# Kernel optimization log

Hardware: AMD Instinct MI355X
Metric: run time of the kernel (lower is better)

The kernel has to match this reference:

```python
import jax, jax.numpy as jnp
import numpy as np

INPUT_DIM, HIDDEN, CB_DIM, CB_SIZE = 768, 512, 256, 512
COMMIT_W = 1.0


def setup_inputs() -> dict:
    key = jax.random.key(0)
    ks = jax.random.split(key, 10)
    def lin(k, fan_in, fan_out):
        lim = 1.0 / np.sqrt(fan_in)
        return jax.random.uniform(k, (fan_in, fan_out), jnp.float32, -lim, lim)
    return {
        "x": jax.random.normal(ks[0], (32, 2048, INPUT_DIM), jnp.float32),
        "W1": lin(ks[1], INPUT_DIM, HIDDEN),
        "b1": jnp.zeros((HIDDEN,), jnp.float32),
        "W2": lin(ks[2], HIDDEN, CB_DIM),
        "b2": jnp.zeros((CB_DIM,), jnp.float32),
        "codebook": jax.random.normal(ks[3], (CB_SIZE, CB_DIM), jnp.float32),
        "W3": lin(ks[4], CB_DIM, HIDDEN),
        "b3": jnp.zeros((HIDDEN,), jnp.float32),
        "W4": lin(ks[5], HIDDEN, INPUT_DIM),
        "b4": jnp.zeros((INPUT_DIM,), jnp.float32),
    }


def reference(x, W1, b1, W2, b2, codebook, W3, b3, W4, b4):
    # encoder MLP: [b, n, 768] -> [b, n, 256]
    h = jax.nn.relu(jnp.einsum('bnd,dh->bnh', x, W1) + b1)
    z = jnp.einsum('bnh,hc->bnc', h, W2) + b2

    # VQ: squared-L2 distance to codebook, argmin, gather
    # d(z, c) = ||z||^2 - 2 z.c + ||c||^2  (||z||^2 constant over argmin, omitted)
    dots = jnp.einsum('bnc,kc->bnk', z, codebook)          # [b, n, K]
    c_sq = jnp.sum(codebook * codebook, axis=-1)            # [K]
    indices = jnp.argmin(c_sq - 2.0 * dots, axis=-1)        # [b, n] int
    q = codebook[indices]                                   # [b, n, 256] gather

    # straight-through estimator + commitment loss
    quantized = z + jax.lax.stop_gradient(q - z)
    commit_loss = COMMIT_W * jnp.mean((z - jax.lax.stop_gradient(q)) ** 2)

    # decoder MLP: [b, n, 256] -> [b, n, 768]
    h2 = jax.nn.relu(jnp.einsum('bnc,ch->bnh', quantized, W3) + b3)
    recon = jnp.einsum('bnh,hd->bnd', h2, W4) + b4
    return recon, indices.astype(jnp.int32), commit_loss
```

## Files before the change

### kernel.cpp

```cpp
#include <hip/hip_runtime.h>

typedef unsigned short u16;
typedef unsigned int   u32;
typedef __attribute__((ext_vector_type(8))) short short8;
typedef __attribute__((ext_vector_type(4))) float f32x4;

#define NTOK 65536
#define IND  768
#define HID  512
#define CBD  256
#define CBS  512

#define OUT_IDX_OFF   ((size_t)NTOK * IND)
#define OUT_LOSS_OFF  (OUT_IDX_OFF + NTOK)

#define OFF_H      ((size_t)0)
#define OFF_Z      ((size_t)134217728)
#define OFF_W1H    ((size_t)201326592)
#define OFF_W1L    ((size_t)202113024)
#define OFF_W2H    ((size_t)202899456)
#define OFF_W2L    ((size_t)203161600)
#define OFF_CBH    ((size_t)203423744)
#define OFF_CBL    ((size_t)203685888)
#define OFF_CSQ    ((size_t)203948032)
#define OFF_PART   ((size_t)0)
#define OFF_TABLE  ((size_t)8388608)
#define OFF_ZSQ    ((size_t)9961472)
#define OFF_IDX    ((size_t)10223616)
#define OFF_FLAGS  ((size_t)10485760)
#define OFF_CNT    ((size_t)10747904)

__device__ __forceinline__ u16 f2bf(float f) {
    u32 u = __float_as_uint(f);
    return (u16)((u + 0x7fffu + ((u >> 16) & 1u)) >> 16);
}
__device__ __forceinline__ float bf2f(u16 h) {
    return __uint_as_float(((u32)h) << 16);
}

__global__ __launch_bounds__(256) void cbsplit(
    const float* __restrict__ cb, u16* __restrict__ hi, u16* __restrict__ lo,
    float* __restrict__ csq)
{
    int c = blockIdx.x, t = threadIdx.x;
    float v = cb[(size_t)c * CBD + t];
    u16 h = f2bf(v); u16 l = f2bf(v - bf2f(h));
    hi[(size_t)c * CBD + t] = h; lo[(size_t)c * CBD + t] = l;
    __shared__ float red[256];
    red[t] = v * v; __syncthreads();
    for (int s = 128; s; s >>= 1) { if (t < s) red[t] += red[t + s]; __syncthreads(); }
    if (!t) csq[c] = red[0];
}

__global__ __launch_bounds__(256) void wsplit(
    const float* __restrict__ W, u16* __restrict__ hi, u16* __restrict__ lo,
    int K, int N)
{
    int n = blockIdx.x;
    for (int k = threadIdx.x; k < K; k += 256) {
        float v = W[(size_t)k * N + n];
        u16 h = f2bf(v); u16 l = f2bf(v - bf2f(h));
        hi[(size_t)n * K + k] = h; lo[(size_t)n * K + k] = l;
    }
}

#define CHS 1040
#define PLN (4 * CHS)

template<int AMODE, int EPI>
__global__ __launch_bounds__(256, 2) void gemm3(
    const float* __restrict__ Af, const u32* __restrict__ Apk,
    const u16* __restrict__ Bhi, const u16* __restrict__ Blo,
    const float* __restrict__ bias,
    u32* __restrict__ Opk, float* __restrict__ Opart,
    int M, int N, int K)
{
    __shared__ u16 lds[4 * PLN];
    u16* sAh = lds;
    u16* sAl = lds + PLN;
    u16* sBh = lds + 2 * PLN;
    u16* sBl = lds + 3 * PLN;
    const int tid  = threadIdx.x;

    const int nwg = gridDim.x * gridDim.y;
    const int hw  = blockIdx.y * gridDim.x + blockIdx.x;
    const int logical = (hw & 7) * (nwg >> 3) + (hw >> 3);
    const int bx = logical % gridDim.x;
    const int by = logical / gridDim.x;

    const int m0 = by * 128, n0 = bx * 128;
    const int w = tid >> 6, lane = tid & 63, quad = lane >> 4, l15 = lane & 15;
    const int wm = (w & 1) * 64, wn = (w >> 1) * 64;

    f32x4 acc[4][4] = {};

    for (int k0 = 0; k0 < K; k0 += 32) {
        __syncthreads();
        if (AMODE == 0) {
            #pragma unroll
            for (int s = 0; s < 4; ++s) {
                int slot = tid + s * 256;
                int m = slot >> 3, kg = (slot & 7) << 2;
                int c = kg >> 3, off = kg & 7;
                float4 v = *(const float4*)(Af + (size_t)(m0 + m) * K + k0 + kg);
                u16 h0 = f2bf(v.x), h1 = f2bf(v.y), h2 = f2bf(v.z), h3 = f2bf(v.w);
                ushort4 hv = {h0, h1, h2, h3};
                ushort4 lv = {f2bf(v.x - bf2f(h0)), f2bf(v.y - bf2f(h1)),
                              f2bf(v.z - bf2f(h2)), f2bf(v.w - bf2f(h3))};
                *(ushort4*)&sAh[c * CHS + m * 8 + off] = hv;
                *(ushort4*)&sAl[c * CHS + m * 8 + off] = lv;
            }
        } else {
            #pragma unroll
            for (int s = 0; s < 4; ++s) {
                int slot = tid + s * 256;
                int m = slot >> 3, ke = (slot & 7) << 2;
                int c = ke >> 3, off = ke & 7;
                uint4 u = *(const uint4*)(Apk + (size_t)(m0 + m) * K + k0 + ke);
                ushort4 hv = {(u16)(u.x & 0xffff), (u16)(u.y & 0xffff),
                              (u16)(u.z & 0xffff), (u16)(u.w & 0xffff)};
                ushort4 lv = {(u16)(u.x >> 16), (u16)(u.y >> 16),
                              (u16)(u.z >> 16), (u16)(u.w >> 16)};
                *(ushort4*)&sAh[c * CHS + m * 8 + off] = hv;
                *(ushort4*)&sAl[c * CHS + m * 8 + off] = lv;
            }
        }
        #pragma unroll
        for (int s = 0; s < 4; ++s) {
            int slot = tid + s * 256;
            int n = (slot & 511) >> 2, ku = slot & 3;
            const u16* src = (slot < 512) ? Bhi : Blo;
            u16* dst = (slot < 512) ? sBh : sBl;
            uint4 u = *(const uint4*)(src + (size_t)(n0 + n) * K + k0 + ku * 8);
            *(uint4*)&dst[ku * CHS + n * 8] = u;
        }
        __syncthreads();

        short8 ah[4], al[4], bh[4], bl[4];
        const int kc = quad * CHS;
        #pragma unroll
        for (int i = 0; i < 4; ++i) {
            int ar = wm + i * 16 + l15;
            int br = wn + i * 16 + l15;
            ah[i] = *(const short8*)&sAh[kc + ar * 8];
            al[i] = *(const short8*)&sAl[kc + ar * 8];
            bh[i] = *(const short8*)&sBh[kc + br * 8];
            bl[i] = *(const short8*)&sBl[kc + br * 8];
        }
        #pragma unroll
        for (int i = 0; i < 4; ++i)
            #pragma unroll
            for (int j = 0; j < 4; ++j) {
                acc[i][j] = __builtin_amdgcn_mfma_f32_16x16x32_bf16(ah[i], bh[j], acc[i][j], 0, 0, 0);
                acc[i][j] = __builtin_amdgcn_mfma_f32_16x16x32_bf16(ah[i], bl[j], acc[i][j], 0, 0, 0);
                acc[i][j] = __builtin_amdgcn_mfma_f32_16x16x32_bf16(al[i], bh[j], acc[i][j], 0, 0, 0);
            }
    }

    if (EPI <= 1) {
        float bn[4];
        #pragma unroll
        for (int j = 0; j < 4; ++j) bn[j] = bias[n0 + wn + j * 16 + l15];
        #pragma unroll
        for (int i = 0; i < 4; ++i)
            #pragma unroll
            for (int r = 0; r < 4; ++r) {
                int row = m0 + wm + i * 16 + quad * 4 + r;
                #pragma unroll
                for (int j = 0; j < 4; ++j) {
                    float v = acc[i][j][r] + bn[j];
                    if (EPI == 0) v = fmaxf(v, 0.f);
                    u16 h = f2bf(v); u16 l = f2bf(v - bf2f(h));
                    Opk[(size_t)row * N + n0 + wn + j * 16 + l15] = (u32)h | ((u32)l << 16);
                }
            }
    } else {
        float cs[4]; int cidx[4];
        #pragma unroll
        for (int j = 0; j < 4; ++j) {
            cidx[j] = n0 + wn + j * 16 + l15;
            cs[j] = bias[cidx[j]];
        }
        const int nparts = gridDim.x * 2;
        const int pslot  = bx * 2 + (w >> 1);
        #pragma unroll
        for (int i = 0; i < 4; ++i)
            #pragma unroll
            for (int r = 0; r < 4; ++r) {
                int row = m0 + wm + i * 16 + quad * 4 + r;
                float d1 = 3.4e38f, d2 = 3.4e38f; int i1 = 0x7fffffff;
                #pragma unroll
                for (int j = 0; j < 4; ++j) {
                    float v = fmaf(-2.0f, acc[i][j][r], cs[j]);
                    if (v < d1) { d2 = d1; d1 = v; i1 = cidx[j]; }
                    else d2 = fminf(d2, v);
                }
                #pragma unroll
                for (int mm = 1; mm < 16; mm <<= 1) {
                    float od1 = __shfl_xor(d1, mm, 64);
                    float od2 = __shfl_xor(d2, mm, 64);
                    int   oi1 = __shfl_xor(i1, mm, 64);
                    if (od1 < d1 || (od1 == d1 && oi1 < i1)) { d2 = fminf(d1, od2); d1 = od1; i1 = oi1; }
                    else d2 = fminf(d2, od1);
                }
                if (l15 == 0) {
                    float4 o = {d1, d2, __int_as_float(i1), 0.f};
                    *(float4*)&Opart[((size_t)row * nparts + pslot) * 4] = o;
                }
            }
    }
}

__global__ __launch_bounds__(256) void zsq_pk(
    const u32* __restrict__ Zpk, float* __restrict__ zsq)
{
    int tok = blockIdx.x * 4 + (threadIdx.x >> 6);
    int lane = threadIdx.x & 63;
    uint4 u = *(const uint4*)(Zpk + (size_t)tok * CBD + lane * 4);
    float z0 = bf2f((u16)(u.x & 0xffff)) + bf2f((u16)(u.x >> 16));
    float z1 = bf2f((u16)(u.y & 0xffff)) + bf2f((u16)(u.y >> 16));
    float z2 = bf2f((u16)(u.z & 0xffff)) + bf2f((u16)(u.z >> 16));
    float z3 = bf2f((u16)(u.w & 0xffff)) + bf2f((u16)(u.w >> 16));
    float s = z0 * z0 + z1 * z1 + z2 * z2 + z3 * z3;
    #pragma unroll
    for (int off = 32; off; off >>= 1) s += __shfl_down(s, off, 64);
    if (!lane) zsq[tok] = s;
}

__global__ __launch_bounds__(256) void vq_reduce(
    const float* __restrict__ part, const float* __restrict__ zsq,
    float* __restrict__ out_idx, int* __restrict__ idx_i,
    int* __restrict__ cnt, float* __restrict__ accum, int* __restrict__ flags)
{
    int tok = blockIdx.x * 256 + threadIdx.x;
    float d1 = 3.4e38f, d2 = 3.4e38f; int i1 = 0x7fffffff;
    #pragma unroll
    for (int nb = 0; nb < 8; ++nb) {
        float4 p = *(const float4*)&part[((size_t)tok * 8 + nb) * 4];
        float pd1 = p.x, pd2 = p.y; int pi1 = __float_as_int(p.z);
        if (pd1 < d1 || (pd1 == d1 && pi1 < i1)) { d2 = fminf(d1, pd2); d1 = pd1; i1 = pi1; }
        else d2 = fminf(d2, pd1);
    }
    out_idx[tok] = (float)i1;
    idx_i[tok] = i1;
    if (d2 - d1 < 0.01f) {
        int p = atomicAdd(cnt, 1);
        if (p >= 0 && p < NTOK) flags[p] = tok;
    }
    float c = zsq[tok] + d1;
    __shared__ float red[256];
    red[threadIdx.x] = c; __syncthreads();
    for (int s = 128; s; s >>= 1) { if (threadIdx.x < s) red[threadIdx.x] += red[threadIdx.x + s]; __syncthreads(); }
    if (!threadIdx.x) atomicAdd(accum, red[0]);
}

__global__ __launch_bounds__(256) void fixup(
    const int* __restrict__ cnt, const int* __restrict__ flags,
    const float* __restrict__ x, const float* __restrict__ W1, const float* __restrict__ b1,
    const float* __restrict__ W2, const float* __restrict__ b2,
    const float* __restrict__ cb, const float* __restrict__ csq,
    int* __restrict__ idx_i, float* __restrict__ out_idx)
{
    __shared__ float xs[8][IND];
    __shared__ float hs[8][HID];
    __shared__ float zs[8][CBD];
    __shared__ float bd_s[4][8];
    __shared__ int   bi_s[4][8];
    __shared__ int   tok_s[8];

    int n = cnt[0]; if (n > NTOK) n = NTOK; if (n < 0) n = 0;
    const int t = threadIdx.x;
    const int nb = (n + 7) >> 3;

    for (int ib = blockIdx.x; ib < nb; ib += gridDim.x) {
        const int base = ib * 8;
        if (t < 8) {
            int fi = base + t; if (fi > n - 1) fi = n - 1;
            tok_s[t] = flags[fi];
        }
        __syncthreads();

        #pragma unroll
        for (int s = 0; s < 6; ++s) {
            int slot = t + s * 256;
            int tt = slot / 192, c4 = slot - tt * 192;
            *(float4*)&xs[tt][c4 * 4] =
                *(const float4*)(x + (size_t)tok_s[tt] * IND + c4 * 4);
        }
        __syncthreads();

        {
            const int tg = t >> 7;
            const int j0 = (t & 127) * 4;
            float a[4][4];
            float4 bb = *(const float4*)(b1 + j0);
            #pragma unroll
            for (int ti = 0; ti < 4; ++ti) {
                a[ti][0] = bb.x; a[ti][1] = bb.y; a[ti][2] = bb.z; a[ti][3] = bb.w;
            }
            for (int k4 = 0; k4 < IND / 4; ++k4) {
                float4 xv[4];
                #pragma unroll
                for (int ti = 0; ti < 4; ++ti)
                    xv[ti] = *(const float4*)&xs[tg * 4 + ti][k4 * 4];
                #pragma unroll
                for (int kk = 0; kk < 4; ++kk) {
                    float4 wv = *(const float4*)(W1 + (size_t)(k4 * 4 + kk) * HID + j0);
                    #pragma unroll
                    for (int ti = 0; ti < 4; ++ti) {
                        float xk = (kk == 0) ? xv[ti].x : (kk == 1) ? xv[ti].y
                                 : (kk == 2) ? xv[ti].z : xv[ti].w;
                        a[ti][0] = fmaf(xk, wv.x, a[ti][0]);
                        a[ti][1] = fmaf(xk, wv.y, a[ti][1]);
                        a[ti][2] = fmaf(xk, wv.z, a[ti][2]);
                        a[ti][3] = fmaf(xk, wv.w, a[ti][3]);
                    }
                }
            }
            #pragma unroll
            for (int ti = 0; ti < 4; ++ti) {
                float4 o = {fmaxf(a[ti][0], 0.f), fmaxf(a[ti][1], 0.f),
                            fmaxf(a[ti][2], 0.f), fmaxf(a[ti][3], 0.f)};
                *(float4*)&hs[tg * 4 + ti][j0] = o;
            }
        }
        __syncthreads();

        {
            const int tg = t >> 6;
            const int c0 = (t & 63) * 4;
            float az[2][4];
            float4 bz = *(const float4*)(b2 + c0);
            #pragma unroll
            for (int ti = 0; ti < 2; ++ti) {
                az[ti][0] = bz.x; az[ti][1] = bz.y; az[ti][2] = bz.z; az[ti][3] = bz.w;
            }
            for (int k4 = 0; k4 < HID / 4; ++k4) {
                float4 hv[2];
                #pragma unroll
                for (int ti = 0; ti < 2; ++ti)
                    hv[ti] = *(const float4*)&hs[tg * 2 + ti][k4 * 4];
                #pragma unroll
                for (int kk = 0; kk < 4; ++kk) {
                    float4 wv = *(const float4*)(W2 + (size_t)(k4 * 4 + kk) * CBD + c0);
                    #pragma unroll
                    for (int ti = 0; ti < 2; ++ti) {
                        float hk = (kk == 0) ? hv[ti].x : (kk == 1) ? hv[ti].y
                                 : (kk == 2) ? hv[ti].z : hv[ti].w;
                        az[ti][0] = fmaf(hk, wv.x, az[ti][0]);
                        az[ti][1] = fmaf(hk, wv.y, az[ti][1]);
                        az[ti][2] = fmaf(hk, wv.z, az[ti][2]);
                        az[ti][3] = fmaf(hk, wv.w, az[ti][3]);
                    }
                }
            }
            #pragma unroll
            for (int ti = 0; ti < 2; ++ti) {
                float4 o = {az[ti][0], az[ti][1], az[ti][2], az[ti][3]};
                *(float4*)&zs[tg * 2 + ti][c0] = o;
            }
        }
        __syncthreads();

        {
            const int wv = t >> 6, l = t & 63;
            float4 zv[8];
            #pragma unroll
            for (int tt = 0; tt < 8; ++tt) zv[tt] = *(const float4*)&zs[tt][l * 4];
            float bd[8]; int bi[8];
            #pragma unroll
            for (int tt = 0; tt < 8; ++tt) { bd[tt] = 3.4e38f; bi[tt] = 0x7fffffff; }
            for (int cc = 0; cc < 128; ++cc) {
                int c = wv * 128 + cc;
                float4 cv = *(const float4*)(cb + (size_t)c * CBD + l * 4);
                float cs = csq[c];
                #pragma unroll
                for (int tt = 0; tt < 8; ++tt) {
                    float p = zv[tt].x * cv.x + zv[tt].y * cv.y + zv[tt].z * cv.z + zv[tt].w * cv.w;
                    #pragma unroll
                    for (int mm = 32; mm; mm >>= 1) p += __shfl_xor(p, mm, 64);
                    float d = cs - 2.f * p;
                    if (d < bd[tt]) { bd[tt] = d; bi[tt] = c; }
                }
            }
            if (l == 0) {
                #pragma unroll
                for (int tt = 0; tt < 8; ++tt) { bd_s[wv][tt] = bd[tt]; bi_s[wv][tt] = bi[tt]; }
            }
        }
        __syncthreads();

        if (t < 8) {
            const int tt = t;
            float d = bd_s[0][tt]; int i = bi_s[0][tt];
            #pragma unroll
            for (int wv = 1; wv < 4; ++wv) {
                float od = bd_s[wv][tt]; int oi = bi_s[wv][tt];
                if (od < d || (od == d && oi < i)) { d = od; i = oi; }
            }
            if (base + tt < n) {
                int tok = tok_s[tt];
                idx_i[tok] = i; out_idx[tok] = (float)i;
            }
        }
        __syncthreads();
    }
}

__global__ __launch_bounds__(256) void table_pre(
    const float* __restrict__ cb, const float* __restrict__ W3,
    const float* __restrict__ b3, const float* __restrict__ W4,
    const float* __restrict__ b4, float* __restrict__ table)
{
    __shared__ float crow[CBD];
    __shared__ float h2[HID];
    const int c = blockIdx.x;
    const int t = threadIdx.x;
    crow[t] = cb[(size_t)c * CBD + t];
    __syncthreads();
    #pragma unroll
    for (int s = 0; s < 2; ++s) {
        int j = t + s * 256;
        float acc = b3[j];
        for (int k = 0; k < CBD; ++k) acc = fmaf(crow[k], W3[(size_t)k * HID + j], acc);
        h2[j] = fmaxf(acc, 0.f);
    }
    __syncthreads();
    #pragma unroll
    for (int s = 0; s < 3; ++s) {
        int j = t + s * 256;
        float acc = b4[j];
        for (int k = 0; k < HID; ++k) acc = fmaf(h2[k], W4[(size_t)k * IND + j], acc);
        table[(size_t)c * IND + j] = acc;
    }
}

__global__ __launch_bounds__(256) void gather_kernel(
    const int* __restrict__ idx, const float* __restrict__ table,
    float* __restrict__ out)
{
    unsigned i = blockIdx.x * 256u + threadIdx.x;
    unsigned tok = i / 192u;
    unsigned c = i - tok * 192u;
    int id = idx[tok];
    ((float4*)out)[i] = ((const float4*)table)[(size_t)id * 192 + c];
}

__global__ void finalize_kernel(const float* __restrict__ accum,
                                float* __restrict__ out_loss)
{
    out_loss[0] = accum[0] * (1.0f / 16777216.0f);
}

extern "C" void kernel_launch(void* const* d_in, const int* in_sizes, int n_in,
                              void* d_out, int out_size, void* d_ws, size_t ws_size,
                              hipStream_t stream) {
    const float* x  = (const float*)d_in[0];
    const float* W1 = (const float*)d_in[1];
    const float* b1 = (const float*)d_in[2];
    const float* W2 = (const float*)d_in[3];
    const float* b2 = (const float*)d_in[4];
    const float* cb = (const float*)d_in[5];
    const float* W3 = (const float*)d_in[6];
    const float* b3 = (const float*)d_in[7];
    const float* W4 = (const float*)d_in[8];
    const float* b4 = (const float*)d_in[9];

    char* ws = (char*)d_ws;
    u32*  Hpk   = (u32*)(ws + OFF_H);
    u32*  Zpk   = (u32*)(ws + OFF_Z);
    u16*  W1h   = (u16*)(ws + OFF_W1H);
    u16*  W1l   = (u16*)(ws + OFF_W1L);
    u16*  W2h   = (u16*)(ws + OFF_W2H);
    u16*  W2l   = (u16*)(ws + OFF_W2L);
    u16*  CBh   = (u16*)(ws + OFF_CBH);
    u16*  CBl   = (u16*)(ws + OFF_CBL);
    float* csq  = (float*)(ws + OFF_CSQ);
    float* part = (float*)(ws + OFF_PART);
    float* table = (float*)(ws + OFF_TABLE);
    float* zsq  = (float*)(ws + OFF_ZSQ);
    int*   idx_i = (int*)(ws + OFF_IDX);
    int*   flags = (int*)(ws + OFF_FLAGS);
    int*   cnt   = (int*)(ws + OFF_CNT);
    float* accum = (float*)(ws + OFF_CNT + 4);

    float* out      = (float*)d_out;
    float* out_idx  = out + OUT_IDX_OFF;
    float* out_loss = out + OUT_LOSS_OFF;

    cbsplit<<<CBS, 256, 0, stream>>>(cb, CBh, CBl, csq);
    wsplit<<<HID, 256, 0, stream>>>(W1, W1h, W1l, IND, HID);
    wsplit<<<CBD, 256, 0, stream>>>(W2, W2h, W2l, HID, CBD);

    gemm3<0, 0><<<dim3(HID / 128, NTOK / 128), 256, 0, stream>>>(
        x, (const u32*)nullptr, W1h, W1l, b1, Hpk, (float*)nullptr, NTOK, HID, IND);
    gemm3<1, 1><<<dim3(CBD / 128, NTOK / 128), 256, 0, stream>>>(
        (const float*)nullptr, Hpk, W2h, W2l, b2, Zpk, (float*)nullptr, NTOK, CBD, HID);

    hipMemsetAsync(cnt, 0, 8, stream);

    zsq_pk<<<NTOK / 4, 256, 0, stream>>>(Zpk, zsq);

    gemm3<1, 2><<<dim3(CBS / 128, NTOK / 128), 256, 0, stream>>>(
        (const float*)nullptr, Zpk, CBh, CBl, csq, (u32*)nullptr, part, NTOK, CBS, CBD);

    table_pre<<<CBS, 256, 0, stream>>>(cb, W3, b3, W4, b4, table);

    vq_reduce<<<NTOK / 256, 256, 0, stream>>>(part, zsq, out_idx, idx_i, cnt, accum, flags);

    fixup<<<1024, 256, 0, stream>>>(cnt, flags, x, W1, b1, W2, b2, cb, csq, idx_i, out_idx);

    gather_kernel<<<(NTOK * (IND / 4)) / 256, 256, 0, stream>>>(idx_i, table, out);

    finalize_kernel<<<1, 1, 0, stream>>>(accum, out_loss);
}
```

Measured before the change: 918.0 us.

## Split packed hi/lo activations into planes and stage GEMM tiles via direct-to-LDS loads

```diff
diff --git a/kernel.cpp b/kernel.cpp
--- a/kernel.cpp
+++ b/kernel.cpp
@@ -14,8 +14,10 @@
 #define OUT_IDX_OFF   ((size_t)NTOK * IND)
 #define OUT_LOSS_OFF  (OUT_IDX_OFF + NTOK)
 
-#define OFF_H      ((size_t)0)
-#define OFF_Z      ((size_t)134217728)
+#define OFF_HH     ((size_t)0)
+#define OFF_HL     ((size_t)67108864)
+#define OFF_ZH     ((size_t)134217728)
+#define OFF_ZL     ((size_t)167772160)
 #define OFF_W1H    ((size_t)201326592)
 #define OFF_W1L    ((size_t)202113024)
 #define OFF_W2H    ((size_t)202899456)
@@ -38,6 +40,12 @@
     return __uint_as_float(((u32)h) << 16);
 }
 
+__device__ __forceinline__ void dma16(const void* g, void* l) {
+    __builtin_amdgcn_global_load_lds(
+        (const __attribute__((address_space(1))) u32*)g,
+        (__attribute__((address_space(3))) u32*)l, 16, 0, 0);
+}
+
 __global__ __launch_bounds__(256) void cbsplit(
     const float* __restrict__ cb, u16* __restrict__ hi, u16* __restrict__ lo,
     float* __restrict__ csq)
@@ -64,22 +72,21 @@
     }
 }
 
-#define CHS 1040
-#define PLN (4 * CHS)
-
 template<int AMODE, int EPI>
 __global__ __launch_bounds__(256, 2) void gemm3(
-    const float* __restrict__ Af, const u32* __restrict__ Apk,
+    const float* __restrict__ Af,
+    const u16* __restrict__ Ahi, const u16* __restrict__ Alo,
     const u16* __restrict__ Bhi, const u16* __restrict__ Blo,
     const float* __restrict__ bias,
-    u32* __restrict__ Opk, float* __restrict__ Opart,
+    u16* __restrict__ Ohi, u16* __restrict__ Olo, float* __restrict__ Opart,
     int M, int N, int K)
 {
-    __shared__ u16 lds[4 * PLN];
+    constexpr int CA = (AMODE == 0) ? 1040 : 1024;
+    __shared__ u16 lds[8 * 1040 + 8 * 1024];
     u16* sAh = lds;
-    u16* sAl = lds + PLN;
-    u16* sBh = lds + 2 * PLN;
-    u16* sBl = lds + 3 * PLN;
+    u16* sAl = lds + 4 * CA;
+    u16* sBh = lds + 8 * CA;
+    u16* sBl = lds + 8 * CA + 4096;
     const int tid  = threadIdx.x;
 
     const int nwg = gridDim.x * gridDim.y;
@@ -96,7 +103,26 @@
 
     for (int k0 = 0; k0 < K; k0 += 32) {
         __syncthreads();
-        if (AMODE == 0) {
+        #pragma unroll
+        for (int g = 0; g < 4; ++g) {
+            int gi = w * 4 + g;
+            int widx = gi & 7;
+            const u16* src = ((gi & 8) ? Blo : Bhi)
+                + (size_t)(n0 + ((widx & 1) << 6) + lane) * K + k0 + ((widx >> 1) << 3);
+            u16* dst = ((gi & 8) ? sBl : sBh) + widx * 512;
+            dma16(src, dst);
+        }
+        if (AMODE == 1) {
+            #pragma unroll
+            for (int g = 0; g < 4; ++g) {
+                int gi = w * 4 + g;
+                int widx = gi & 7;
+                const u16* src = ((gi & 8) ? Alo : Ahi)
+                    + (size_t)(m0 + ((widx & 1) << 6) + lane) * K + k0 + ((widx >> 1) << 3);
+                u16* dst = ((gi & 8) ? sAl : sAh) + widx * 512;
+                dma16(src, dst);
+            }
+        } else {
             #pragma unroll
             for (int s = 0; s < 4; ++s) {
                 int slot = tid + s * 256;
@@ -107,45 +133,21 @@
                 ushort4 hv = {h0, h1, h2, h3};
                 ushort4 lv = {f2bf(v.x - bf2f(h0)), f2bf(v.y - bf2f(h1)),
                               f2bf(v.z - bf2f(h2)), f2bf(v.w - bf2f(h3))};
-                *(ushort4*)&sAh[c * CHS + m * 8 + off] = hv;
-                *(ushort4*)&sAl[c * CHS + m * 8 + off] = lv;
-            }
-        } else {
-            #pragma unroll
-            for (int s = 0; s < 4; ++s) {
-                int slot = tid + s * 256;
-                int m = slot >> 3, ke = (slot & 7) << 2;
-                int c = ke >> 3, off = ke & 7;
-                uint4 u = *(const uint4*)(Apk + (size_t)(m0 + m) * K + k0 + ke);
-                ushort4 hv = {(u16)(u.x & 0xffff), (u16)(u.y & 0xffff),
-                              (u16)(u.z & 0xffff), (u16)(u.w & 0xffff)};
-                ushort4 lv = {(u16)(u.x >> 16), (u16)(u.y >> 16),
-                              (u16)(u.z >> 16), (u16)(u.w >> 16)};
-                *(ushort4*)&sAh[c * CHS + m * 8 + off] = hv;
-                *(ushort4*)&sAl[c * CHS + m * 8 + off] = lv;
-            }
-        }
-        #pragma unroll
-        for (int s = 0; s < 4; ++s) {
-            int slot = tid + s * 256;
-            int n = (slot & 511) >> 2, ku = slot & 3;
-            const u16* src = (slot < 512) ? Bhi : Blo;
-            u16* dst = (slot < 512) ? sBh : sBl;
-            uint4 u = *(const uint4*)(src + (size_t)(n0 + n) * K + k0 + ku * 8);
-            *(uint4*)&dst[ku * CHS + n * 8] = u;
+                *(ushort4*)&sAh[c * CA + m * 8 + off] = hv;
+                *(ushort4*)&sAl[c * CA + m * 8 + off] = lv;
+            }
         }
         __syncthreads();
 
         short8 ah[4], al[4], bh[4], bl[4];
-        const int kc = quad * CHS;
         #pragma unroll
         for (int i = 0; i < 4; ++i) {
             int ar = wm + i * 16 + l15;
             int br = wn + i * 16 + l15;
-            ah[i] = *(const short8*)&sAh[kc + ar * 8];
-            al[i] = *(const short8*)&sAl[kc + ar * 8];
-            bh[i] = *(const short8*)&sBh[kc + br * 8];
-            bl[i] = *(const short8*)&sBl[kc + br * 8];
+            ah[i] = *(const short8*)&sAh[quad * CA + ar * 8];
+            al[i] = *(const short8*)&sAl[quad * CA + ar * 8];
+            bh[i] = *(const short8*)&sBh[quad * 1024 + br * 8];
+            bl[i] = *(const short8*)&sBl[quad * 1024 + br * 8];
         }
         #pragma unroll
         for (int i = 0; i < 4; ++i)
@@ -171,7 +173,8 @@
                     float v = acc[i][j][r] + bn[j];
                     if (EPI == 0) v = fmaxf(v, 0.f);
                     u16 h = f2bf(v); u16 l = f2bf(v - bf2f(h));
-                    Opk[(size_t)row * N + n0 + wn + j * 16 + l15] = (u32)h | ((u32)l << 16);
+                    size_t o = (size_t)row * N + n0 + wn + j * 16 + l15;
+                    Ohi[o] = h; Olo[o] = l;
                 }
             }
     } else {
@@ -212,15 +215,16 @@
 }
 
 __global__ __launch_bounds__(256) void zsq_pk(
-    const u32* __restrict__ Zpk, float* __restrict__ zsq)
+    const u16* __restrict__ Zh, const u16* __restrict__ Zl, float* __restrict__ zsq)
 {
     int tok = blockIdx.x * 4 + (threadIdx.x >> 6);
     int lane = threadIdx.x & 63;
-    uint4 u = *(const uint4*)(Zpk + (size_t)tok * CBD + lane * 4);
-    float z0 = bf2f((u16)(u.x & 0xffff)) + bf2f((u16)(u.x >> 16));
-    float z1 = bf2f((u16)(u.y & 0xffff)) + bf2f((u16)(u.y >> 16));
-    float z2 = bf2f((u16)(u.z & 0xffff)) + bf2f((u16)(u.z >> 16));
-    float z3 = bf2f((u16)(u.w & 0xffff)) + bf2f((u16)(u.w >> 16));
+    ushort4 uh = *(const ushort4*)(Zh + (size_t)tok * CBD + lane * 4);
+    ushort4 ul = *(const ushort4*)(Zl + (size_t)tok * CBD + lane * 4);
+    float z0 = bf2f(uh.x) + bf2f(ul.x);
+    float z1 = bf2f(uh.y) + bf2f(ul.y);
+    float z2 = bf2f(uh.z) + bf2f(ul.z);
+    float z3 = bf2f(uh.w) + bf2f(ul.w);
     float s = z0 * z0 + z1 * z1 + z2 * z2 + z3 * z3;
     #pragma unroll
     for (int off = 32; off; off >>= 1) s += __shfl_down(s, off, 64);
@@ -264,21 +268,44 @@
     __shared__ float xs[8][IND];
     __shared__ float hs[8][HID];
     __shared__ float zs[8][CBD];
+    __shared__ float wbuf[2][2048];
+    __shared__ float csq_s[CBS];
     __shared__ float bd_s[4][8];
     __shared__ int   bi_s[4][8];
     __shared__ int   tok_s[8];
 
     int n = cnt[0]; if (n > NTOK) n = NTOK; if (n < 0) n = 0;
     const int t = threadIdx.x;
+    const int w = t >> 6, lane = t & 63;
     const int nb = (n + 7) >> 3;
+
+    if (t < 128) *(float4*)&csq_s[t * 4] = *(const float4*)(csq + t * 4);
+
+    auto stage_w1 = [&](int ch, int p) {
+        #pragma unroll
+        for (int g = 0; g < 2; ++g) {
+            int gi = w * 2 + g;
+            dma16(W1 + (size_t)ch * 2048 + gi * 256 + lane * 4, &wbuf[p][gi * 256]);
+        }
+    };
+    auto stage_w2 = [&](int ch, int p) {
+        #pragma unroll
+        for (int g = 0; g < 2; ++g) {
+            int gi = w * 2 + g;
+            dma16(W2 + (size_t)ch * 2048 + gi * 256 + lane * 4, &wbuf[p][gi * 256]);
+        }
+    };
 
     for (int ib = blockIdx.x; ib < nb; ib += gridDim.x) {
         const int base = ib * 8;
+        __syncthreads();
         if (t < 8) {
             int fi = base + t; if (fi > n - 1) fi = n - 1;
             tok_s[t] = flags[fi];
         }
         __syncthreads();
+
+        stage_w1(0, 0);
 
         #pragma unroll
         for (int s = 0; s < 6; ++s) {
@@ -287,7 +314,6 @@
             *(float4*)&xs[tt][c4 * 4] =
                 *(const float4*)(x + (size_t)tok_s[tt] * IND + c4 * 4);
         }
-        __syncthreads();
 
         {
             const int tg = t >> 7;
@@ -298,14 +324,16 @@
             for (int ti = 0; ti < 4; ++ti) {
                 a[ti][0] = bb.x; a[ti][1] = bb.y; a[ti][2] = bb.z; a[ti][3] = bb.w;
             }
-            for (int k4 = 0; k4 < IND / 4; ++k4) {
+            for (int ch = 0; ch < 192; ++ch) {
+                __syncthreads();
+                if (ch + 1 < 192) stage_w1(ch + 1, (ch + 1) & 1);
                 float4 xv[4];
                 #pragma unroll
                 for (int ti = 0; ti < 4; ++ti)
-                    xv[ti] = *(const float4*)&xs[tg * 4 + ti][k4 * 4];
+                    xv[ti] = *(const float4*)&xs[tg * 4 + ti][ch * 4];
                 #pragma unroll
                 for (int kk = 0; kk < 4; ++kk) {
-                    float4 wv = *(const float4*)(W1 + (size_t)(k4 * 4 + kk) * HID + j0);
+                    float4 wv = *(const float4*)&wbuf[ch & 1][kk * 512 + j0];
                     #pragma unroll
                     for (int ti = 0; ti < 4; ++ti) {
                         float xk = (kk == 0) ? xv[ti].x : (kk == 1) ? xv[ti].y
@@ -335,22 +363,28 @@
             for (int ti = 0; ti < 2; ++ti) {
                 az[ti][0] = bz.x; az[ti][1] = bz.y; az[ti][2] = bz.z; az[ti][3] = bz.w;
             }
-            for (int k4 = 0; k4 < HID / 4; ++k4) {
-                float4 hv[2];
-                #pragma unroll
-                for (int ti = 0; ti < 2; ++ti)
-                    hv[ti] = *(const float4*)&hs[tg * 2 + ti][k4 * 4];
-                #pragma unroll
-                for (int kk = 0; kk < 4; ++kk) {
-                    float4 wv = *(const float4*)(W2 + (size_t)(k4 * 4 + kk) * CBD + c0);
+            stage_w2(0, 0);
+            for (int ch = 0; ch < 64; ++ch) {
+                __syncthreads();
+                if (ch + 1 < 64) stage_w2(ch + 1, (ch + 1) & 1);
+                #pragma unroll
+                for (int k4 = 0; k4 < 2; ++k4) {
+                    float4 hv[2];
                     #pragma unroll
-                    for (int ti = 0; ti < 2; ++ti) {
-                        float hk = (kk == 0) ? hv[ti].x : (kk == 1) ? hv[ti].y
-                                 : (kk == 2) ? hv[ti].z : hv[ti].w;
-                        az[ti][0] = fmaf(hk, wv.x, az[ti][0]);
-                        az[ti][1] = fmaf(hk, wv.y, az[ti][1]);
-                        az[ti][2] = fmaf(hk, wv.z, az[ti][2]);
-                        az[ti][3] = fmaf(hk, wv.w, az[ti][3]);
+                    for (int ti = 0; ti < 2; ++ti)
+                        hv[ti] = *(const float4*)&hs[tg * 2 + ti][ch * 8 + k4 * 4];
+                    #pragma unroll
+                    for (int kk = 0; kk < 4; ++kk) {
+                        float4 wv = *(const float4*)&wbuf[ch & 1][(k4 * 4 + kk) * 256 + c0];
+                        #pragma unroll
+                        for (int ti = 0; ti < 2; ++ti) {
+                            float hk = (kk == 0) ? hv[ti].x : (kk == 1) ? hv[ti].y
+                                     : (kk == 2) ? hv[ti].z : hv[ti].w;
+                            az[ti][0] = fmaf(hk, wv.x, az[ti][0]);
+                            az[ti][1] = fmaf(hk, wv.y, az[ti][1]);
+                            az[ti][2] = fmaf(hk, wv.z, az[ti][2]);
+                            az[ti][3] = fmaf(hk, wv.w, az[ti][3]);
+                        }
                     }
                 }
             }
@@ -373,7 +407,7 @@
             for (int cc = 0; cc < 128; ++cc) {
                 int c = wv * 128 + cc;
                 float4 cv = *(const float4*)(cb + (size_t)c * CBD + l * 4);
-                float cs = csq[c];
+                float cs = csq_s[c];
                 #pragma unroll
                 for (int tt = 0; tt < 8; ++tt) {
                     float p = zv[tt].x * cv.x + zv[tt].y * cv.y + zv[tt].z * cv.z + zv[tt].w * cv.w;
@@ -403,7 +437,6 @@
                 idx_i[tok] = i; out_idx[tok] = (float)i;
             }
         }
-        __syncthreads();
     }
 }
 
@@ -467,8 +500,10 @@
     const float* b4 = (const float*)d_in[9];
 
     char* ws = (char*)d_ws;
-    u32*  Hpk   = (u32*)(ws + OFF_H);
-    u32*  Zpk   = (u32*)(ws + OFF_Z);
+    u16*  Hh    = (u16*)(ws + OFF_HH);
+    u16*  Hl    = (u16*)(ws + OFF_HL);
+    u16*  Zh    = (u16*)(ws + OFF_ZH);
+    u16*  Zl    = (u16*)(ws + OFF_ZL);
     u16*  W1h   = (u16*)(ws + OFF_W1H);
     u16*  W1l   = (u16*)(ws + OFF_W1L);
     u16*  W2h   = (u16*)(ws + OFF_W2H);
@@ -493,16 +528,19 @@
     wsplit<<<CBD, 256, 0, stream>>>(W2, W2h, W2l, HID, CBD);
 
     gemm3<0, 0><<<dim3(HID / 128, NTOK / 128), 256, 0, stream>>>(
-        x, (const u32*)nullptr, W1h, W1l, b1, Hpk, (float*)nullptr, NTOK, HID, IND);
+        x, (const u16*)nullptr, (const u16*)nullptr, W1h, W1l, b1,
+        Hh, Hl, (float*)nullptr, NTOK, HID, IND);
     gemm3<1, 1><<<dim3(CBD / 128, NTOK / 128), 256, 0, stream>>>(
-        (const float*)nullptr, Hpk, W2h, W2l, b2, Zpk, (float*)nullptr, NTOK, CBD, HID);
+        (const float*)nullptr, Hh, Hl, W2h, W2l, b2,
+        Zh, Zl, (float*)nullptr, NTOK, CBD, HID);
 
     hipMemsetAsync(cnt, 0, 8, stream);
 
-    zsq_pk<<<NTOK / 4, 256, 0, stream>>>(Zpk, zsq);
+    zsq_pk<<<NTOK / 4, 256, 0, stream>>>(Zh, Zl, zsq);
 
     gemm3<1, 2><<<dim3(CBS / 128, NTOK / 128), 256, 0, stream>>>(
-        (const float*)nullptr, Zpk, CBh, CBl, csq, (u32*)nullptr, part, NTOK, CBS, CBD);
+        (const float*)nullptr, Zh, Zl, CBh, CBl, csq,
+        (u16*)nullptr, (u16*)nullptr, part, NTOK, CBS, CBD);
 
     table_pre<<<CBS, 256, 0, stream>>>(cb, W3, b3, W4, b4, table);
 
```

Result: slower. 1.092 ms (+19.0%).

## Software-pipeline weight loads and remap codebook distance loop in fixup kernel

Applied to the files above, without the earlier changes.

```diff
diff --git a/kernel.cpp b/kernel.cpp
--- a/kernel.cpp
+++ b/kernel.cpp
@@ -254,6 +254,27 @@
     if (!threadIdx.x) atomicAdd(accum, red[0]);
 }
 
+__device__ __forceinline__ void fma16(float (&a)[4][4],
+    float x0, float x1, float x2, float x3, float4 w)
+{
+    a[0][0] = fmaf(x0, w.x, a[0][0]); a[0][1] = fmaf(x0, w.y, a[0][1]);
+    a[0][2] = fmaf(x0, w.z, a[0][2]); a[0][3] = fmaf(x0, w.w, a[0][3]);
+    a[1][0] = fmaf(x1, w.x, a[1][0]); a[1][1] = fmaf(x1, w.y, a[1][1]);
+    a[1][2] = fmaf(x1, w.z, a[1][2]); a[1][3] = fmaf(x1, w.w, a[1][3]);
+    a[2][0] = fmaf(x2, w.x, a[2][0]); a[2][1] = fmaf(x2, w.y, a[2][1]);
+    a[2][2] = fmaf(x2, w.z, a[2][2]); a[2][3] = fmaf(x2, w.w, a[2][3]);
+    a[3][0] = fmaf(x3, w.x, a[3][0]); a[3][1] = fmaf(x3, w.y, a[3][1]);
+    a[3][2] = fmaf(x3, w.z, a[3][2]); a[3][3] = fmaf(x3, w.w, a[3][3]);
+}
+__device__ __forceinline__ void fma8(float (&a)[2][4],
+    float x0, float x1, float4 w)
+{
+    a[0][0] = fmaf(x0, w.x, a[0][0]); a[0][1] = fmaf(x0, w.y, a[0][1]);
+    a[0][2] = fmaf(x0, w.z, a[0][2]); a[0][3] = fmaf(x0, w.w, a[0][3]);
+    a[1][0] = fmaf(x1, w.x, a[1][0]); a[1][1] = fmaf(x1, w.y, a[1][1]);
+    a[1][2] = fmaf(x1, w.z, a[1][2]); a[1][3] = fmaf(x1, w.w, a[1][3]);
+}
+
 __global__ __launch_bounds__(256) void fixup(
     const int* __restrict__ cnt, const int* __restrict__ flags,
     const float* __restrict__ x, const float* __restrict__ W1, const float* __restrict__ b1,
@@ -264,6 +285,7 @@
     __shared__ float xs[8][IND];
     __shared__ float hs[8][HID];
     __shared__ float zs[8][CBD];
+    __shared__ float csq_s[CBS];
     __shared__ float bd_s[4][8];
     __shared__ int   bi_s[4][8];
     __shared__ int   tok_s[8];
@@ -272,8 +294,11 @@
     const int t = threadIdx.x;
     const int nb = (n + 7) >> 3;
 
+    if (t < 128) *(float4*)&csq_s[t * 4] = *(const float4*)(csq + t * 4);
+
     for (int ib = blockIdx.x; ib < nb; ib += gridDim.x) {
         const int base = ib * 8;
+        __syncthreads();
         if (t < 8) {
             int fi = base + t; if (fi > n - 1) fi = n - 1;
             tok_s[t] = flags[fi];
@@ -290,7 +315,7 @@
         __syncthreads();
 
         {
-            const int tg = t >> 7;
+            const int tg4 = (t >> 7) * 4;
             const int j0 = (t & 127) * 4;
             float a[4][4];
             float4 bb = *(const float4*)(b1 + j0);
@@ -298,36 +323,43 @@
             for (int ti = 0; ti < 4; ++ti) {
                 a[ti][0] = bb.x; a[ti][1] = bb.y; a[ti][2] = bb.z; a[ti][3] = bb.w;
             }
-            for (int k4 = 0; k4 < IND / 4; ++k4) {
-                float4 xv[4];
-                #pragma unroll
-                for (int ti = 0; ti < 4; ++ti)
-                    xv[ti] = *(const float4*)&xs[tg * 4 + ti][k4 * 4];
-                #pragma unroll
-                for (int kk = 0; kk < 4; ++kk) {
-                    float4 wv = *(const float4*)(W1 + (size_t)(k4 * 4 + kk) * HID + j0);
-                    #pragma unroll
-                    for (int ti = 0; ti < 4; ++ti) {
-                        float xk = (kk == 0) ? xv[ti].x : (kk == 1) ? xv[ti].y
-                                 : (kk == 2) ? xv[ti].z : xv[ti].w;
-                        a[ti][0] = fmaf(xk, wv.x, a[ti][0]);
-                        a[ti][1] = fmaf(xk, wv.y, a[ti][1]);
-                        a[ti][2] = fmaf(xk, wv.z, a[ti][2]);
-                        a[ti][3] = fmaf(xk, wv.w, a[ti][3]);
-                    }
-                }
-            }
+            const float* Wb = W1 + j0;
+#define LW1(s, K4) { const int _k = (((K4) < 192) ? (K4) : 191) * 2048;        \
+            s##0 = *(const float4*)(Wb + _k);                                  \
+            s##1 = *(const float4*)(Wb + _k + 512);                            \
+            s##2 = *(const float4*)(Wb + _k + 1024);                           \
+            s##3 = *(const float4*)(Wb + _k + 1536); }
+#define CMP1(s, K4) {                                                          \
+            float4 xv0 = *(const float4*)&xs[tg4 + 0][(K4) * 4];               \
+            float4 xv1 = *(const float4*)&xs[tg4 + 1][(K4) * 4];               \
+            float4 xv2 = *(const float4*)&xs[tg4 + 2][(K4) * 4];               \
+            float4 xv3 = *(const float4*)&xs[tg4 + 3][(K4) * 4];               \
+            fma16(a, xv0.x, xv1.x, xv2.x, xv3.x, s##0);                        \
+            fma16(a, xv0.y, xv1.y, xv2.y, xv3.y, s##1);                        \
+            fma16(a, xv0.z, xv1.z, xv2.z, xv3.z, s##2);                        \
+            fma16(a, xv0.w, xv1.w, xv2.w, xv3.w, s##3); }
+            float4 wA0, wA1, wA2, wA3, wB0, wB1, wB2, wB3;
+            float4 wC0, wC1, wC2, wC3, wD0, wD1, wD2, wD3;
+            LW1(wA, 0); LW1(wB, 1); LW1(wC, 2);
+            for (int k4 = 0; k4 < 192; k4 += 4) {
+                LW1(wD, k4 + 3); CMP1(wA, k4 + 0);
+                LW1(wA, k4 + 4); CMP1(wB, k4 + 1);
+                LW1(wB, k4 + 5); CMP1(wC, k4 + 2);
+                LW1(wC, k4 + 6); CMP1(wD, k4 + 3);
+            }
+#undef LW1
+#undef CMP1
             #pragma unroll
             for (int ti = 0; ti < 4; ++ti) {
                 float4 o = {fmaxf(a[ti][0], 0.f), fmaxf(a[ti][1], 0.f),
                             fmaxf(a[ti][2], 0.f), fmaxf(a[ti][3], 0.f)};
-                *(float4*)&hs[tg * 4 + ti][j0] = o;
+                *(float4*)&hs[tg4 + ti][j0] = o;
             }
         }
         __syncthreads();
 
         {
-            const int tg = t >> 6;
+            const int tg2 = (t >> 6) * 2;
             const int c0 = (t & 63) * 4;
             float az[2][4];
             float4 bz = *(const float4*)(b2 + c0);
@@ -335,52 +367,77 @@
             for (int ti = 0; ti < 2; ++ti) {
                 az[ti][0] = bz.x; az[ti][1] = bz.y; az[ti][2] = bz.z; az[ti][3] = bz.w;
             }
-            for (int k4 = 0; k4 < HID / 4; ++k4) {
-                float4 hv[2];
-                #pragma unroll
-                for (int ti = 0; ti < 2; ++ti)
-                    hv[ti] = *(const float4*)&hs[tg * 2 + ti][k4 * 4];
-                #pragma unroll
-                for (int kk = 0; kk < 4; ++kk) {
-                    float4 wv = *(const float4*)(W2 + (size_t)(k4 * 4 + kk) * CBD + c0);
-                    #pragma unroll
-                    for (int ti = 0; ti < 2; ++ti) {
-                        float hk = (kk == 0) ? hv[ti].x : (kk == 1) ? hv[ti].y
-                                 : (kk == 2) ? hv[ti].z : hv[ti].w;
-                        az[ti][0] = fmaf(hk, wv.x, az[ti][0]);
-                        az[ti][1] = fmaf(hk, wv.y, az[ti][1]);
-                        az[ti][2] = fmaf(hk, wv.z, az[ti][2]);
-                        az[ti][3] = fmaf(hk, wv.w, az[ti][3]);
-                    }
-                }
-            }
+            const float* Wb = W2 + c0;
+#define LW2(s, K4) { const int _k = (((K4) < 128) ? (K4) : 127) * 1024;        \
+            s##0 = *(const float4*)(Wb + _k);                                  \
+            s##1 = *(const float4*)(Wb + _k + 256);                            \
+            s##2 = *(const float4*)(Wb + _k + 512);                            \
+            s##3 = *(const float4*)(Wb + _k + 768); }
+#define CMP2(s, K4) {                                                          \
+            float4 hv0 = *(const float4*)&hs[tg2 + 0][(K4) * 4];               \
+            float4 hv1 = *(const float4*)&hs[tg2 + 1][(K4) * 4];               \
+            fma8(az, hv0.x, hv1.x, s##0);                                      \
+            fma8(az, hv0.y, hv1.y, s##1);                                      \
+            fma8(az, hv0.z, hv1.z, s##2);                                      \
+            fma8(az, hv0.w, hv1.w, s##3); }
+            float4 wA0, wA1, wA2, wA3, wB0, wB1, wB2, wB3;
+            float4 wC0, wC1, wC2, wC3, wD0, wD1, wD2, wD3;
+            LW2(wA, 0); LW2(wB, 1); LW2(wC, 2);
+            for (int k4 = 0; k4 < 128; k4 += 4) {
+                LW2(wD, k4 + 3); CMP2(wA, k4 + 0);
+                LW2(wA, k4 + 4); CMP2(wB, k4 + 1);
+                LW2(wB, k4 + 5); CMP2(wC, k4 + 2);
+                LW2(wC, k4 + 6); CMP2(wD, k4 + 3);
+            }
+#undef LW2
+#undef CMP2
             #pragma unroll
             for (int ti = 0; ti < 2; ++ti) {
                 float4 o = {az[ti][0], az[ti][1], az[ti][2], az[ti][3]};
-                *(float4*)&zs[tg * 2 + ti][c0] = o;
+                *(float4*)&zs[tg2 + ti][c0] = o;
             }
         }
         __syncthreads();
 
         {
             const int wv = t >> 6, l = t & 63;
-            float4 zv[8];
-            #pragma unroll
-            for (int tt = 0; tt < 8; ++tt) zv[tt] = *(const float4*)&zs[tt][l * 4];
-            float bd[8]; int bi[8];
-            #pragma unroll
-            for (int tt = 0; tt < 8; ++tt) { bd[tt] = 3.4e38f; bi[tt] = 0x7fffffff; }
-            for (int cc = 0; cc < 128; ++cc) {
-                int c = wv * 128 + cc;
-                float4 cv = *(const float4*)(cb + (size_t)c * CBD + l * 4);
-                float cs = csq[c];
+            const float* cb0 = cb + (size_t)t * CBD;
+            const float* cb1 = cb + (size_t)(t + 256) * CBD;
+            float d0[8], d1[8];
+            #pragma unroll
+            for (int tt = 0; tt < 8; ++tt) { d0[tt] = 0.f; d1[tt] = 0.f; }
+            float4 pA = *(const float4*)(cb0);
+            float4 pB = *(const float4*)(cb1);
+            for (int k4 = 0; k4 < 64; ++k4) {
+                float4 cA = pA, cB = pB;
+                int kn = (k4 + 1 < 64) ? (k4 + 1) : 63;
+                pA = *(const float4*)(cb0 + kn * 4);
+                pB = *(const float4*)(cb1 + kn * 4);
                 #pragma unroll
                 for (int tt = 0; tt < 8; ++tt) {
-                    float p = zv[tt].x * cv.x + zv[tt].y * cv.y + zv[tt].z * cv.z + zv[tt].w * cv.w;
-                    #pragma unroll
-                    for (int mm = 32; mm; mm >>= 1) p += __shfl_xor(p, mm, 64);
-                    float d = cs - 2.f * p;
-                    if (d < bd[tt]) { bd[tt] = d; bi[tt] = c; }
+                    float4 zv = *(const float4*)&zs[tt][k4 * 4];
+                    d0[tt] = fmaf(zv.w, cA.w, fmaf(zv.z, cA.z,
+                             fmaf(zv.y, cA.y, fmaf(zv.x, cA.x, d0[tt]))));
+                    d1[tt] = fmaf(zv.w, cB.w, fmaf(zv.z, cB.z,
+                             fmaf(zv.y, cB.y, fmaf(zv.x, cB.x, d1[tt]))));
+                }
+            }
+            float bd[8]; int bi[8];
+            const float cs0 = csq_s[t], cs1 = csq_s[t + 256];
+            #pragma unroll
+            for (int tt = 0; tt < 8; ++tt) {
+                float e0 = cs0 - 2.f * d0[tt];
+                float e1 = cs1 - 2.f * d1[tt];
+                if (e0 <= e1) { bd[tt] = e0; bi[tt] = t; }
+                else          { bd[tt] = e1; bi[tt] = t + 256; }
+            }
+            #pragma unroll
+            for (int mm = 1; mm < 64; mm <<= 1) {
+                #pragma unroll
+                for (int tt = 0; tt < 8; ++tt) {
+                    float od = __shfl_xor(bd[tt], mm, 64);
+                    int   oi = __shfl_xor(bi[tt], mm, 64);
+                    if (od < bd[tt] || (od == bd[tt] && oi < bi[tt])) { bd[tt] = od; bi[tt] = oi; }
                 }
             }
             if (l == 0) {
```

Measured after the change: 972.9 us. +6.0%, slower.
